# Performance work log

Hardware: AMD Instinct MI355X
Metric: run time of the kernel (lower is better)

## Reference

```python
import jax, jax.numpy as jnp
import numpy as np

N_HEAD = 8
HID = 256
V_DIM = HID // N_HEAD
IN_CH = 3
OUT_CH = 1
N_BLOCKS = 4
BATCH = 4
N_FULL = 4096
N_LAT = 1024
LOCALITIES = (3.0, 5.0, 5.0, 5.0, 5.0, 3.0)


def _linear(x, w, b):
    # eqx.nn.Linear convention: w is [out, in]
    return x @ w.T + b


def _pos_att(m_dist, x, r, weight, locality):
    # m_dist: [h, Nq, Nk]; x: [b, Nk, HID]; r: [h,1,1]; weight: [h, HID, V_DIM]
    scale = jnp.tan(0.25 * jnp.pi * (1 - 1e-07) * (1 + jnp.sin(r)))  # [h,1,1]
    sd = m_dist * scale  # [h, Nq, Nk]
    if locality <= 100:
        thr = jnp.percentile(sd, locality, axis=-1, keepdims=True)
        sd = jnp.where(sd <= thr, sd, jnp.inf)
    att = jax.nn.softmax(-sd, axis=-1)  # [h, Nq, Nk]
    value = jnp.einsum('bnj,hjk->bhnk', x, weight)  # [b, h, Nk, V_DIM]
    out = jnp.einsum('hjn,bhnk->bhjk', att, value)  # [b, h, Nq, V_DIM]
    out = out.transpose(0, 2, 1, 3).reshape(out.shape[0], out.shape[2], -1)  # [b, Nq, HID]
    return jax.nn.gelu(out)


def setup_inputs():
    key = jax.random.key(0)
    ks = jax.random.split(key, 16)
    def nrm(k, shape, scale=1.0):
        return jax.random.normal(k, shape, dtype=jnp.float32) * scale
    inv = float(1.0 / np.sqrt(HID))
    return {
        'x': nrm(ks[0], (BATCH, N_FULL, IN_CH)),
        'm_dist_down': jax.random.uniform(ks[1], (N_HEAD, N_LAT, N_FULL), dtype=jnp.float32),
        'm_dist_blocks': jax.random.uniform(ks[2], (N_BLOCKS, N_HEAD, N_LAT, N_LAT), dtype=jnp.float32),
        'm_dist_up': jax.random.uniform(ks[3], (N_HEAD, N_FULL, N_LAT), dtype=jnp.float32),
        'en_w': nrm(ks[4], (HID, IN_CH), float(1.0 / np.sqrt(IN_CH))),
        'en_b': jnp.zeros((HID,), jnp.float32),
        'down_r': nrm(ks[5], (N_HEAD, 1, 1)),
        'down_w': nrm(ks[6], (N_HEAD, HID, V_DIM), inv),
        'pa_r': nrm(ks[7], (N_BLOCKS, N_HEAD, 1, 1)),
        'pa_w': nrm(ks[8], (N_BLOCKS, N_HEAD, HID, V_DIM), inv),
        'mlp1_w': nrm(ks[9], (N_BLOCKS, HID, HID), inv),
        'mlp1_b': jnp.zeros((N_BLOCKS, HID), jnp.float32),
        'mlp2_w': nrm(ks[10], (N_BLOCKS, HID, HID), inv),
        'mlp2_b': jnp.zeros((N_BLOCKS, HID), jnp.float32),
        'res_w': nrm(ks[11], (N_BLOCKS, HID, HID), inv),
        'res_b': jnp.zeros((N_BLOCKS, HID), jnp.float32),
        'up_r': nrm(ks[12], (N_HEAD, 1, 1)),
        'up_w': nrm(ks[13], (N_HEAD, HID, V_DIM), inv),
        'de1_w': nrm(ks[14], (HID, HID), inv),
        'de1_b': jnp.zeros((HID,), jnp.float32),
        'de2_w': nrm(ks[15], (OUT_CH, HID), inv),
        'de2_b': jnp.zeros((OUT_CH,), jnp.float32),
    }


def reference(x, m_dist_down, m_dist_blocks, m_dist_up, en_w, en_b, down_r, down_w,
              pa_r, pa_w, mlp1_w, mlp1_b, mlp2_w, mlp2_b, res_w, res_b,
              up_r, up_w, de1_w, de1_b, de2_w, de2_b):
    # Encoder: lift + downsampling position-attention
    h = jax.nn.gelu(_linear(x, en_w, en_b))  # [b, N_FULL, HID]
    h = _pos_att(m_dist_down, h, down_r, down_w, LOCALITIES[0])  # [b, N_LAT, HID]
    # Processor blocks: PA -> MLP, plus linear residual, gelu
    for i in range(N_BLOCKS):
        pa = _pos_att(m_dist_blocks[i], h, pa_r[i], pa_w[i], LOCALITIES[1 + i])
        mlp = _linear(jax.nn.gelu(_linear(pa, mlp1_w[i], mlp1_b[i])), mlp2_w[i], mlp2_b[i])
        h = jax.nn.gelu(mlp + _linear(h, res_w[i], res_b[i]))
    # Decoder: upsampling position-attention + projection
    h = _pos_att(m_dist_up, h, up_r, up_w, LOCALITIES[-1])  # [b, N_FULL, HID]
    h = jax.nn.gelu(_linear(h, de1_w, de1_b))
    return _linear(h, de2_w, de2_b)  # [b, N_FULL, OUT_CH]
```

## Files before the change

kernel.cpp:

```cpp
#include <hip/hip_runtime.h>
#include <math.h>


typedef short bf16x8 __attribute__((ext_vector_type(8)));
typedef float f32x4 __attribute__((ext_vector_type(4)));

__device__ __forceinline__ float gelu_f(float x) {
  float x3 = x * x * x;
  float inner = x + 0.044715f * x3;
  float t = tanhf(0.7978845608028654f * inner);
  return x * (0.5f * (1.0f + t));
}

__device__ __forceinline__ unsigned short f2bf(float x) {
  union { float f; unsigned u; } v; v.f = x;
  return (unsigned short)((v.u + 0x7fffu + ((v.u >> 16) & 1u)) >> 16);
}
__device__ __forceinline__ float bf2f(unsigned short b) {
  union { unsigned u; float f; } v; v.u = ((unsigned)b) << 16; return v.f;
}
__device__ __forceinline__ void store_bf(unsigned short* hi, unsigned short* lo,
                                         size_t i, float v) {
  unsigned short h = f2bf(v);
  hi[i] = h;
  lo[i] = f2bf(v - bf2f(h));
}

struct PrepArgs {
  const float *mlp1, *mlp2, *res, *de1, *down, *pa, *up;
  const float *down_r, *pa_r, *up_r;
  unsigned short *rm_hi, *rm_lo, *val_hi, *val_lo;
  float* scales;
};
__global__ __launch_bounds__(256) void k_prep(PrepArgs p) {
  if (blockIdx.x == 4864) {
    int t = threadIdx.x;
    if (t >= 48) return;
    float rv;
    if (t < 8) rv = p.down_r[t];
    else if (t < 40) rv = p.pa_r[t - 8];
    else rv = p.up_r[t - 40];
    double rd = (double)rv;
    float s1 = (float)sin(rd);
    float u = 1.0f + s1;
    float vc = (float)(0.7853981633974483 * (1.0 - 1e-7));
    float wf = vc * u;
    p.scales[t] = (float)tan((double)wf);
    return;
  }
  int i = blockIdx.x * 256 + threadIdx.x;
  if (i < 851968) {
    const float* src; int off;
    if (i < 262144)      { src = p.mlp1; off = i; }
    else if (i < 524288) { src = p.mlp2; off = i - 262144; }
    else if (i < 786432) { src = p.res;  off = i - 524288; }
    else                 { src = p.de1;  off = i - 786432; }
    float x = src[off];
    store_bf(p.rm_hi, p.rm_lo, i, x);
  } else if (i < 1245184) {
    int ii = i - 851968;
    const float* src; int off;
    if (ii < 65536)       { src = p.down; off = ii; }
    else if (ii < 327680) { src = p.pa;   off = ii - 65536; }
    else                  { src = p.up;   off = ii - 327680; }
    int m = off >> 16, rem = off & 65535;
    int o = rem >> 8, j = rem & 255;
    float x = src[(size_t)m * 65536 + (o >> 5) * 8192 + j * 32 + (o & 31)];
    store_bf(p.val_hi, p.val_lo, ii, x);
  }
}

__global__ __launch_bounds__(256) void k_lift(const float* __restrict__ x,
                                              const float* __restrict__ w,
                                              const float* __restrict__ b,
                                              unsigned short* __restrict__ ohi,
                                              unsigned short* __restrict__ olo) {
  int gid = blockIdx.x * 256 + threadIdx.x;
  int m = gid >> 8, o = gid & 255;
  float a0 = x[m * 3 + 0], a1 = x[m * 3 + 1], a2 = x[m * 3 + 2];
  float acc = a0 * w[o * 3 + 0] + a1 * w[o * 3 + 1] + a2 * w[o * 3 + 2] + b[o];
  store_bf(ohi, olo, gid, gelu_f(acc));
}

template <int ACT, int ADDRES, int OBF16>
__global__ __launch_bounds__(256) void k_gemm(
    const unsigned short* __restrict__ Ahi, const unsigned short* __restrict__ Alo,
    const unsigned short* __restrict__ Whi, const unsigned short* __restrict__ Wlo,
    const float* __restrict__ bias, const float* __restrict__ D,
    float* __restrict__ C, unsigned short* __restrict__ Chi,
    unsigned short* __restrict__ Clo) {
  int t = threadIdx.x;
  int w = t >> 6, l = t & 63;
  int m0 = blockIdx.x * 64 + (w >> 1) * 32;
  int o0 = blockIdx.y * 64 + (w & 1) * 32;
  int fr = l & 15, fq = l >> 4;
  f32x4 acc[2][2] = {};
  size_t a0 = (size_t)(m0 + fr) * 256 + fq * 8;
  size_t a1 = a0 + 16 * 256;
  size_t b0 = (size_t)(o0 + fr) * 256 + fq * 8;
  size_t b1 = b0 + 16 * 256;
  for (int ks = 0; ks < 8; ++ks) {
    int k0 = ks * 32;
    bf16x8 A0h = *(const bf16x8*)(Ahi + a0 + k0);
    bf16x8 A0l = *(const bf16x8*)(Alo + a0 + k0);
    bf16x8 A1h = *(const bf16x8*)(Ahi + a1 + k0);
    bf16x8 A1l = *(const bf16x8*)(Alo + a1 + k0);
    bf16x8 B0h = *(const bf16x8*)(Whi + b0 + k0);
    bf16x8 B0l = *(const bf16x8*)(Wlo + b0 + k0);
    bf16x8 B1h = *(const bf16x8*)(Whi + b1 + k0);
    bf16x8 B1l = *(const bf16x8*)(Wlo + b1 + k0);
#define MFMA4(ACC, AH, AL, BH, BL)                                            \
  ACC = __builtin_amdgcn_mfma_f32_16x16x32_bf16(AH, BH, ACC, 0, 0, 0);        \
  ACC = __builtin_amdgcn_mfma_f32_16x16x32_bf16(AH, BL, ACC, 0, 0, 0);        \
  ACC = __builtin_amdgcn_mfma_f32_16x16x32_bf16(AL, BH, ACC, 0, 0, 0);        \
  ACC = __builtin_amdgcn_mfma_f32_16x16x32_bf16(AL, BL, ACC, 0, 0, 0);
    MFMA4(acc[0][0], A0h, A0l, B0h, B0l)
    MFMA4(acc[0][1], A0h, A0l, B1h, B1l)
    MFMA4(acc[1][0], A1h, A1l, B0h, B0l)
    MFMA4(acc[1][1], A1h, A1l, B1h, B1l)
#undef MFMA4
  }
  float bb[2];
  bb[0] = bias ? bias[o0 + fr] : 0.0f;
  bb[1] = bias ? bias[o0 + 16 + fr] : 0.0f;
#pragma unroll
  for (int i = 0; i < 2; ++i) {
#pragma unroll
    for (int jx = 0; jx < 2; ++jx) {
      int col = o0 + jx * 16 + fr;
#pragma unroll
      for (int r = 0; r < 4; ++r) {
        int rowi = m0 + i * 16 + fq * 4 + r;
        size_t oidx = (size_t)rowi * 256 + col;
        float v = acc[i][jx][r] + bb[jx];
        if (ADDRES) v += D[oidx];
        if (ACT) v = gelu_f(v);
        if (OBF16) store_bf(Chi, Clo, oidx, v);
        else C[oidx] = v;
      }
    }
  }
}

template <int N, int CAP, int MW>
__global__ __launch_bounds__(256, MW) void k_wselpv(
    const float* __restrict__ mdist, const float* __restrict__ scales,
    int sc_off, int Nq, int k_lo, float hw, float lw, float frac,
    const float* __restrict__ V, int Nk,
    unsigned short* __restrict__ out_hi, unsigned short* __restrict__ out_lo) {
  constexpr int CH = N / 256;
  constexpr int SMAX = (CAP + 63) / 64;
  __shared__ float cv[4][CAP];
  __shared__ int ci[4][CAP];
  __shared__ int ccnt[4];
  __shared__ float svsel[4][2];
  __shared__ float swin[4][32];

  int tid = threadIdx.x;
  int w = tid >> 6, l = tid & 63;
  int row = blockIdx.x * 4 + w;
  int h = row / Nq, j = row - h * Nq;
  float scale = scales[sc_off + h];
  const float4* mrow4 = (const float4*)(mdist + (size_t)row * N);

  float lmin = INFINITY, lmax = -INFINITY;
#pragma unroll
  for (int e = 0; e < CH; ++e) {
    float4 v = mrow4[l + 64 * e];
    lmin = fminf(lmin, fminf(fminf(v.x, v.y), fminf(v.z, v.w)));
    lmax = fmaxf(lmax, fmaxf(fmaxf(v.x, v.y), fmaxf(v.z, v.w)));
  }
#pragma unroll
  for (int off = 32; off > 0; off >>= 1) {
    lmin = fminf(lmin, __shfl_xor(lmin, off));
    lmax = fmaxf(lmax, __shfl_xor(lmax, off));
  }
  float rmin = lmin, rmax = lmax;

  int K = 0;
  float inv_total = 1.0f;
  if (rmax > rmin) {
    float range = rmax - rmin;
    float margin = fmaxf(fabsf(rmax) * 1e-6f, 1e-30f);
    float rtop = rmax + margin;
    float wtop = rmin + range * frac;
    if (!(wtop > rmin)) wtop = rtop;
    float v_lo = rmin, v_hi = rmin;
    int count = 0;
    float xv[SMAX];
    for (int it = 0; it < 20; ++it) {
      if (l == 0) ccnt[w] = 0;
#pragma unroll
      for (int e = 0; e < CH; ++e) {
        float4 v = mrow4[l + 64 * e];
        int i0 = 4 * (l + 64 * e);
        if (v.x < wtop) { int p = atomicAdd(&ccnt[w], 1); if (p < CAP) { cv[w][p] = v.x; ci[w][p] = i0; } }
        if (v.y < wtop) { int p = atomicAdd(&ccnt[w], 1); if (p < CAP) { cv[w][p] = v.y; ci[w][p] = i0 + 1; } }
        if (v.z < wtop) { int p = atomicAdd(&ccnt[w], 1); if (p < CAP) { cv[w][p] = v.z; ci[w][p] = i0 + 2; } }
        if (v.w < wtop) { int p = atomicAdd(&ccnt[w], 1); if (p < CAP) { cv[w][p] = v.w; ci[w][p] = i0 + 3; } }
      }
      count = ccnt[w];
      if (count < k_lo + 2) { wtop = fminf(rmin + (wtop - rmin) * 3.0f, rtop); continue; }
      if (count > CAP)      { wtop = rmin + (wtop - rmin) * 0.6f; continue; }

#pragma unroll
      for (int s = 0; s < SMAX; ++s) {
        int slot = l + 64 * s;
        xv[s] = (slot < count) ? cv[w][slot] : INFINITY;
      }
      float wlo = rmin, whi = wtop;
      int rbase = 0, cntw = count;
      int found = 0, degen = 0;
      for (int bs = 0; bs < 32; ++bs) {
        if (cntw <= 24) break;
        float mid = 0.5f * (wlo + whi);
        if (!(mid > wlo && mid < whi)) { degen = 1; break; }
        int c4 = 0;
#pragma unroll
        for (int s = 0; s < SMAX; ++s) c4 += (xv[s] >= wlo && xv[s] < mid) ? 1 : 0;
#pragma unroll
        for (int off = 32; off > 0; off >>= 1) c4 += __shfl_xor(c4, off);
        int rrel = k_lo - rbase;
        if (rrel + 1 < c4) { whi = mid; cntw = c4; }
        else if (rrel >= c4) { wlo = mid; rbase += c4; cntw -= c4; }
        else {
          float mx = -INFINITY, mn = INFINITY;
#pragma unroll
          for (int s = 0; s < SMAX; ++s) {
            float v = xv[s];
            if (v >= wlo && v < mid) mx = fmaxf(mx, v);
            if (v >= mid && v < whi) mn = fminf(mn, v);
          }
#pragma unroll
          for (int off = 32; off > 0; off >>= 1) {
            mx = fmaxf(mx, __shfl_xor(mx, off));
            mn = fminf(mn, __shfl_xor(mn, off));
          }
          v_lo = mx; v_hi = mn; found = 1;
          break;
        }
      }
      if (!found) {
        if (!degen && cntw <= 32) {
          if (l == 0) ccnt[w] = 0;
#pragma unroll
          for (int s = 0; s < SMAX; ++s) {
            float v = xv[s];
            if (v >= wlo && v < whi) {
              int p = atomicAdd(&ccnt[w], 1);
              if (p < 32) swin[w][p] = v;
            }
          }
          int m = ccnt[w];
          if (m > 32) m = 32;
          float myv = (l < m) ? swin[w][l] : INFINITY;
          int clt = 0, ceq = 0;
          for (int jj = 0; jj < m; ++jj) {
            float y = swin[w][jj];
            clt += (y < myv) ? 1 : 0;
            ceq += (y == myv) ? 1 : 0;
          }
          int rr = k_lo - rbase;
          if (l < m) {
            if (clt <= rr && rr < clt + ceq) svsel[w][0] = myv;
            if (clt <= rr + 1 && rr + 1 < clt + ceq) svsel[w][1] = myv;
          }
          v_lo = svsel[w][0];
          v_hi = svsel[w][1];
        } else {
          int clt[SMAX], ceq[SMAX];
#pragma unroll
          for (int s = 0; s < SMAX; ++s) { clt[s] = 0; ceq[s] = 0; }
          for (int jj = 0; jj < count; ++jj) {
            float y = cv[w][jj];
#pragma unroll
            for (int s = 0; s < SMAX; ++s) {
              clt[s] += (y < xv[s]) ? 1 : 0;
              ceq[s] += (y == xv[s]) ? 1 : 0;
            }
          }
#pragma unroll
          for (int s = 0; s < SMAX; ++s) {
            int slot = l + 64 * s;
            if (slot < count) {
              if (clt[s] <= k_lo && k_lo < clt[s] + ceq[s]) svsel[w][0] = xv[s];
              if (clt[s] <= k_lo + 1 && k_lo + 1 < clt[s] + ceq[s]) svsel[w][1] = xv[s];
            }
          }
          v_lo = svsel[w][0];
          v_hi = svsel[w][1];
        }
      }
      float vlos0 = __fmul_rn(v_lo, scale);
      float vhis0 = __fmul_rn(v_hi, scale);
      float thr0 = __fadd_rn(__fmul_rn(vlos0, lw), __fmul_rn(vhis0, hw));
      if (__fmul_rn(wtop, scale) <= thr0) {
        wtop = fminf(rmin + (wtop - rmin) * 3.0f, rtop);
        continue;
      }
      break;
    }

    float vlos = __fmul_rn(v_lo, scale);
    float vhis = __fmul_rn(v_hi, scale);
    float thr = __fadd_rn(__fmul_rn(vlos, lw), __fmul_rn(vhis, hw));
    float rmins = __fmul_rn(rmin, scale);

    int oi[SMAX]; int kp[SMAX];
#pragma unroll
    for (int s = 0; s < SMAX; ++s) {
      int slot = l + 64 * s;
      oi[s] = 0; kp[s] = 0;
      if (slot < count) {
        oi[s] = ci[w][slot];
        kp[s] = (__fmul_rn(xv[s], scale) <= thr) ? 1 : 0;
      }
    }
    int base = 0;
    float lsum = 0.0f;
    unsigned long long mlt = (l == 0) ? 0ull : (~0ull >> (64 - l));
#pragma unroll
    for (int s = 0; s < SMAX; ++s) {
      unsigned long long bal = __ballot(kp[s] != 0);
      int pos = base + (int)__popcll(bal & mlt);
      if (kp[s]) {
        float e0 = expf(__fsub_rn(rmins, __fmul_rn(xv[s], scale)));
        cv[w][pos] = e0;
        ci[w][pos] = oi[s];
        lsum += e0;
      }
      base += (int)__popcll(bal);
    }
    K = base;
#pragma unroll
    for (int off = 32; off > 0; off >>= 1) lsum += __shfl_xor(lsum, off);
    inv_total = 1.0f / lsum;
  } else {
    K = 0;
    inv_total = 1.0f / (float)Nk;
  }

  int b = l >> 4, c4 = (l & 15) * 2;
  int hcol = h * 32 + c4;
  const float* Vb = V + (size_t)b * Nk * 256;
  float acc0 = 0.0f, acc1 = 0.0f;
  if (K > 0) {
    for (int e = 0; e < K; ++e) {
      float we = cv[w][e];
      int n = ci[w][e];
      const float2 vv = *(const float2*)(Vb + (size_t)n * 256 + hcol);
      acc0 = fmaf(we, vv.x, acc0);
      acc1 = fmaf(we, vv.y, acc1);
    }
  } else {
    for (int n = 0; n < Nk; ++n) {
      const float2 vv = *(const float2*)(Vb + (size_t)n * 256 + hcol);
      acc0 += vv.x;
      acc1 += vv.y;
    }
  }
  size_t oidx = ((size_t)b * Nq + j) * 256 + hcol;
  store_bf(out_hi, out_lo, oidx, gelu_f(acc0 * inv_total));
  store_bf(out_hi, out_lo, oidx + 1, gelu_f(acc1 * inv_total));
}

__global__ __launch_bounds__(256) void k_de2(const float* __restrict__ A,
                                             const float* __restrict__ w,
                                             const float* __restrict__ b,
                                             float* __restrict__ out) {
  int t = threadIdx.x;
  int row = blockIdx.x * 4 + (t >> 6);
  int lane = t & 63;
  const float* ar = A + (size_t)row * 256;
  float s = 0.0f;
  for (int i = lane; i < 256; i += 64) s = fmaf(ar[i], w[i], s);
#pragma unroll
  for (int off = 32; off > 0; off >>= 1) s += __shfl_down(s, off);
  if (lane == 0) out[row] = s + b[0];
}

struct SelParams { int k_lo; float hw, lw, frac; };
static SelParams sel_params(double q, int N) {
  SelParams p;
  float idx_q = (float)(q / 100.0);
  float pos = idx_q * (float)(N - 1);
  float lo = floorf(pos);
  p.k_lo = (int)lo;
  p.hw = pos - lo;
  p.lw = 1.0f - p.hw;
  float need = (float)(p.k_lo + 2);
  p.frac = (need + 6.0f * sqrtf(need) + 8.0f) / (float)N;
  return p;
}

extern "C" void kernel_launch(void* const* d_in, const int* in_sizes, int n_in,
                              void* d_out, int out_size, void* d_ws, size_t ws_size,
                              hipStream_t stream) {
  const float* x      = (const float*)d_in[0];
  const float* mdd    = (const float*)d_in[1];
  const float* mdb    = (const float*)d_in[2];
  const float* mdu    = (const float*)d_in[3];
  const float* en_w   = (const float*)d_in[4];
  const float* en_b   = (const float*)d_in[5];
  const float* down_r = (const float*)d_in[6];
  const float* down_w = (const float*)d_in[7];
  const float* pa_r   = (const float*)d_in[8];
  const float* pa_w   = (const float*)d_in[9];
  const float* mlp1_w = (const float*)d_in[10];
  const float* mlp1_b = (const float*)d_in[11];
  const float* mlp2_w = (const float*)d_in[12];
  const float* mlp2_b = (const float*)d_in[13];
  const float* res_w  = (const float*)d_in[14];
  const float* res_b  = (const float*)d_in[15];
  const float* up_r   = (const float*)d_in[16];
  const float* up_w   = (const float*)d_in[17];
  const float* de1_w  = (const float*)d_in[18];
  const float* de1_b  = (const float*)d_in[19];
  const float* de2_w  = (const float*)d_in[20];
  const float* de2_b  = (const float*)d_in[21];
  float* out = (float*)d_out;
  char* base = (char*)d_ws;

  float* val               = (float*)base;
  float* t2                = (float*)(base + 16777216);
  unsigned short* hfull_hi = (unsigned short*)(base + 20971520);
  unsigned short* hfull_lo = (unsigned short*)(base + 29360128);
  unsigned short* paout_hi = (unsigned short*)(base + 37748736);
  unsigned short* paout_lo = (unsigned short*)(base + 46137344);
  unsigned short* hlat_hi  = (unsigned short*)(base + 54525952);
  unsigned short* hlat_lo  = (unsigned short*)(base + 56623104);
  unsigned short* t1_hi    = (unsigned short*)(base + 58720256);
  unsigned short* t1_lo    = (unsigned short*)(base + 60817408);
  unsigned short* wrm_hi   = (unsigned short*)(base + 62914560);
  unsigned short* wrm_lo   = (unsigned short*)(base + 64618496);
  unsigned short* wval_hi  = (unsigned short*)(base + 66322432);
  unsigned short* wval_lo  = (unsigned short*)(base + 67108864);
  float* scales            = (float*)(base + 67895296);

  PrepArgs pa;
  pa.mlp1 = mlp1_w; pa.mlp2 = mlp2_w; pa.res = res_w; pa.de1 = de1_w;
  pa.down = down_w; pa.pa = pa_w; pa.up = up_w;
  pa.down_r = down_r; pa.pa_r = pa_r; pa.up_r = up_r;
  pa.rm_hi = wrm_hi; pa.rm_lo = wrm_lo; pa.val_hi = wval_hi; pa.val_lo = wval_lo;
  pa.scales = scales;
  k_prep<<<4865, 256, 0, stream>>>(pa);

  k_lift<<<16384, 256, 0, stream>>>(x, en_w, en_b, hfull_hi, hfull_lo);

  SelParams pd = sel_params(3.0, 4096);
  k_gemm<0, 0, 0><<<dim3(256, 4), 256, 0, stream>>>(
      hfull_hi, hfull_lo, wval_hi, wval_lo, nullptr, nullptr, val, nullptr, nullptr);
  k_wselpv<4096, 256, 4><<<2048, 256, 0, stream>>>(
      mdd, scales, 0, 1024, pd.k_lo, pd.hw, pd.lw, pd.frac, val, 4096, hlat_hi, hlat_lo);

  SelParams pb = sel_params(5.0, 1024);
  for (int i = 0; i < 4; i++) {
    k_gemm<0, 0, 0><<<dim3(64, 4), 256, 0, stream>>>(
        hlat_hi, hlat_lo, wval_hi + 65536 + i * 65536, wval_lo + 65536 + i * 65536,
        nullptr, nullptr, val, nullptr, nullptr);
    k_wselpv<1024, 256, 8><<<2048, 256, 0, stream>>>(
        mdb + (size_t)i * 8388608, scales, 8 + i * 8, 1024, pb.k_lo, pb.hw, pb.lw,
        pb.frac, val, 1024, paout_hi, paout_lo);
    k_gemm<1, 0, 1><<<dim3(64, 4), 256, 0, stream>>>(
        paout_hi, paout_lo, wrm_hi + i * 65536, wrm_lo + i * 65536,
        mlp1_b + i * 256, nullptr, nullptr, t1_hi, t1_lo);
    k_gemm<0, 0, 0><<<dim3(64, 4), 256, 0, stream>>>(
        hlat_hi, hlat_lo, wrm_hi + 524288 + i * 65536, wrm_lo + 524288 + i * 65536,
        res_b + i * 256, nullptr, t2, nullptr, nullptr);
    k_gemm<1, 1, 1><<<dim3(64, 4), 256, 0, stream>>>(
        t1_hi, t1_lo, wrm_hi + 262144 + i * 65536, wrm_lo + 262144 + i * 65536,
        mlp2_b + i * 256, t2, nullptr, hlat_hi, hlat_lo);
  }

  SelParams pu = sel_params(3.0, 1024);
  k_gemm<0, 0, 0><<<dim3(64, 4), 256, 0, stream>>>(
      hlat_hi, hlat_lo, wval_hi + 327680, wval_lo + 327680, nullptr, nullptr,
      val, nullptr, nullptr);
  k_wselpv<1024, 192, 8><<<8192, 256, 0, stream>>>(
      mdu, scales, 40, 4096, pu.k_lo, pu.hw, pu.lw, pu.frac, val, 1024,
      paout_hi, paout_lo);

  k_gemm<1, 0, 0><<<dim3(256, 4), 256, 0, stream>>>(
      paout_hi, paout_lo, wrm_hi + 786432, wrm_lo + 786432, de1_b, nullptr,
      val, nullptr, nullptr);
  k_de2<<<4096, 256, 0, stream>>>(val, de2_w, de2_b, out);
}
```

Measured before the change: 566.7 us.

## Fuse residual and MLP2 GEMMs; merge min/max scan with candidate collection in selection

Result: faster. 521.7 us (-8.0%).

```diff
diff --git a/kernel.cpp b/kernel.cpp
--- a/kernel.cpp
+++ b/kernel.cpp
@@ -99,6 +99,11 @@
   size_t a1 = a0 + 16 * 256;
   size_t b0 = (size_t)(o0 + fr) * 256 + fq * 8;
   size_t b1 = b0 + 16 * 256;
+#define MFMA4(ACC, AH, AL, BH, BL)                                            \
+  ACC = __builtin_amdgcn_mfma_f32_16x16x32_bf16(AH, BH, ACC, 0, 0, 0);        \
+  ACC = __builtin_amdgcn_mfma_f32_16x16x32_bf16(AH, BL, ACC, 0, 0, 0);        \
+  ACC = __builtin_amdgcn_mfma_f32_16x16x32_bf16(AL, BH, ACC, 0, 0, 0);        \
+  ACC = __builtin_amdgcn_mfma_f32_16x16x32_bf16(AL, BL, ACC, 0, 0, 0);
   for (int ks = 0; ks < 8; ++ks) {
     int k0 = ks * 32;
     bf16x8 A0h = *(const bf16x8*)(Ahi + a0 + k0);
@@ -109,16 +114,10 @@
     bf16x8 B0l = *(const bf16x8*)(Wlo + b0 + k0);
     bf16x8 B1h = *(const bf16x8*)(Whi + b1 + k0);
     bf16x8 B1l = *(const bf16x8*)(Wlo + b1 + k0);
-#define MFMA4(ACC, AH, AL, BH, BL)                                            \
-  ACC = __builtin_amdgcn_mfma_f32_16x16x32_bf16(AH, BH, ACC, 0, 0, 0);        \
-  ACC = __builtin_amdgcn_mfma_f32_16x16x32_bf16(AH, BL, ACC, 0, 0, 0);        \
-  ACC = __builtin_amdgcn_mfma_f32_16x16x32_bf16(AL, BH, ACC, 0, 0, 0);        \
-  ACC = __builtin_amdgcn_mfma_f32_16x16x32_bf16(AL, BL, ACC, 0, 0, 0);
     MFMA4(acc[0][0], A0h, A0l, B0h, B0l)
     MFMA4(acc[0][1], A0h, A0l, B1h, B1l)
     MFMA4(acc[1][0], A1h, A1l, B0h, B0l)
     MFMA4(acc[1][1], A1h, A1l, B1h, B1l)
-#undef MFMA4
   }
   float bb[2];
   bb[0] = bias ? bias[o0 + fr] : 0.0f;
@@ -137,6 +136,73 @@
         if (ACT) v = gelu_f(v);
         if (OBF16) store_bf(Chi, Clo, oidx, v);
         else C[oidx] = v;
+      }
+    }
+  }
+}
+
+__global__ __launch_bounds__(256) void k_gemm2(
+    const unsigned short* __restrict__ A1hi, const unsigned short* __restrict__ A1lo,
+    const unsigned short* __restrict__ W1hi, const unsigned short* __restrict__ W1lo,
+    const unsigned short* __restrict__ A2hi, const unsigned short* __restrict__ A2lo,
+    const unsigned short* __restrict__ W2hi, const unsigned short* __restrict__ W2lo,
+    const float* __restrict__ b1, const float* __restrict__ b2,
+    unsigned short* __restrict__ Chi, unsigned short* __restrict__ Clo) {
+  int t = threadIdx.x;
+  int w = t >> 6, l = t & 63;
+  int m0 = blockIdx.x * 64 + (w >> 1) * 32;
+  int o0 = blockIdx.y * 64 + (w & 1) * 32;
+  int fr = l & 15, fq = l >> 4;
+  f32x4 acc[2][2] = {};
+  size_t a0 = (size_t)(m0 + fr) * 256 + fq * 8;
+  size_t a1 = a0 + 16 * 256;
+  size_t b0 = (size_t)(o0 + fr) * 256 + fq * 8;
+  size_t b1o = b0 + 16 * 256;
+  for (int ks = 0; ks < 8; ++ks) {
+    int k0 = ks * 32;
+    {
+      bf16x8 A0h = *(const bf16x8*)(A1hi + a0 + k0);
+      bf16x8 A0l = *(const bf16x8*)(A1lo + a0 + k0);
+      bf16x8 A1h_ = *(const bf16x8*)(A1hi + a1 + k0);
+      bf16x8 A1l_ = *(const bf16x8*)(A1lo + a1 + k0);
+      bf16x8 B0h = *(const bf16x8*)(W1hi + b0 + k0);
+      bf16x8 B0l = *(const bf16x8*)(W1lo + b0 + k0);
+      bf16x8 B1h = *(const bf16x8*)(W1hi + b1o + k0);
+      bf16x8 B1l = *(const bf16x8*)(W1lo + b1o + k0);
+      MFMA4(acc[0][0], A0h, A0l, B0h, B0l)
+      MFMA4(acc[0][1], A0h, A0l, B1h, B1l)
+      MFMA4(acc[1][0], A1h_, A1l_, B0h, B0l)
+      MFMA4(acc[1][1], A1h_, A1l_, B1h, B1l)
+    }
+    {
+      bf16x8 A0h = *(const bf16x8*)(A2hi + a0 + k0);
+      bf16x8 A0l = *(const bf16x8*)(A2lo + a0 + k0);
+      bf16x8 A1h_ = *(const bf16x8*)(A2hi + a1 + k0);
+      bf16x8 A1l_ = *(const bf16x8*)(A2lo + a1 + k0);
+      bf16x8 B0h = *(const bf16x8*)(W2hi + b0 + k0);
+      bf16x8 B0l = *(const bf16x8*)(W2lo + b0 + k0);
+      bf16x8 B1h = *(const bf16x8*)(W2hi + b1o + k0);
+      bf16x8 B1l = *(const bf16x8*)(W2lo + b1o + k0);
+      MFMA4(acc[0][0], A0h, A0l, B0h, B0l)
+      MFMA4(acc[0][1], A0h, A0l, B1h, B1l)
+      MFMA4(acc[1][0], A1h_, A1l_, B0h, B0l)
+      MFMA4(acc[1][1], A1h_, A1l_, B1h, B1l)
+    }
+  }
+#undef MFMA4
+  float bb[2];
+  bb[0] = b1[o0 + fr] + b2[o0 + fr];
+  bb[1] = b1[o0 + 16 + fr] + b2[o0 + 16 + fr];
+#pragma unroll
+  for (int i = 0; i < 2; ++i) {
+#pragma unroll
+    for (int jx = 0; jx < 2; ++jx) {
+      int col = o0 + jx * 16 + fr;
+#pragma unroll
+      for (int r = 0; r < 4; ++r) {
+        int rowi = m0 + i * 16 + fq * 4 + r;
+        size_t oidx = (size_t)rowi * 256 + col;
+        store_bf(Chi, Clo, oidx, gelu_f(acc[i][jx][r] + bb[jx]));
       }
     }
   }
@@ -163,12 +229,28 @@
   float scale = scales[sc_off + h];
   const float4* mrow4 = (const float4*)(mdist + (size_t)row * N);
 
+  float4 s0 = mrow4[l];
+  float smin = fminf(fminf(s0.x, s0.y), fminf(s0.z, s0.w));
+  float smax = fmaxf(fmaxf(s0.x, s0.y), fmaxf(s0.z, s0.w));
+#pragma unroll
+  for (int off = 32; off > 0; off >>= 1) {
+    smin = fminf(smin, __shfl_xor(smin, off));
+    smax = fmaxf(smax, __shfl_xor(smax, off));
+  }
+  float est = smin + (smax - smin) * frac;
+
+  if (l == 0) ccnt[w] = 0;
   float lmin = INFINITY, lmax = -INFINITY;
-#pragma unroll
+#pragma unroll 4
   for (int e = 0; e < CH; ++e) {
     float4 v = mrow4[l + 64 * e];
     lmin = fminf(lmin, fminf(fminf(v.x, v.y), fminf(v.z, v.w)));
     lmax = fmaxf(lmax, fmaxf(fmaxf(v.x, v.y), fmaxf(v.z, v.w)));
+    int i0 = 4 * (l + 64 * e);
+    if (v.x < est) { int p = atomicAdd(&ccnt[w], 1); if (p < CAP) { cv[w][p] = v.x; ci[w][p] = i0; } }
+    if (v.y < est) { int p = atomicAdd(&ccnt[w], 1); if (p < CAP) { cv[w][p] = v.y; ci[w][p] = i0 + 1; } }
+    if (v.z < est) { int p = atomicAdd(&ccnt[w], 1); if (p < CAP) { cv[w][p] = v.z; ci[w][p] = i0 + 2; } }
+    if (v.w < est) { int p = atomicAdd(&ccnt[w], 1); if (p < CAP) { cv[w][p] = v.w; ci[w][p] = i0 + 3; } }
   }
 #pragma unroll
   for (int off = 32; off > 0; off >>= 1) {
@@ -183,25 +265,44 @@
     float range = rmax - rmin;
     float margin = fmaxf(fabsf(rmax) * 1e-6f, 1e-30f);
     float rtop = rmax + margin;
-    float wtop = rmin + range * frac;
-    if (!(wtop > rmin)) wtop = rtop;
+    float wtop = est;
+    bool have = true;
+    if (!(wtop > rmin)) {
+      wtop = rmin + range * frac;
+      if (!(wtop > rmin)) wtop = rtop;
+      have = false;
+    }
+    int attempt = 0;
     float v_lo = rmin, v_hi = rmin;
     int count = 0;
     float xv[SMAX];
     for (int it = 0; it < 20; ++it) {
-      if (l == 0) ccnt[w] = 0;
-#pragma unroll
-      for (int e = 0; e < CH; ++e) {
-        float4 v = mrow4[l + 64 * e];
-        int i0 = 4 * (l + 64 * e);
-        if (v.x < wtop) { int p = atomicAdd(&ccnt[w], 1); if (p < CAP) { cv[w][p] = v.x; ci[w][p] = i0; } }
-        if (v.y < wtop) { int p = atomicAdd(&ccnt[w], 1); if (p < CAP) { cv[w][p] = v.y; ci[w][p] = i0 + 1; } }
-        if (v.z < wtop) { int p = atomicAdd(&ccnt[w], 1); if (p < CAP) { cv[w][p] = v.z; ci[w][p] = i0 + 2; } }
-        if (v.w < wtop) { int p = atomicAdd(&ccnt[w], 1); if (p < CAP) { cv[w][p] = v.w; ci[w][p] = i0 + 3; } }
+      if (!have) {
+        if (l == 0) ccnt[w] = 0;
+#pragma unroll 4
+        for (int e = 0; e < CH; ++e) {
+          float4 v = mrow4[l + 64 * e];
+          int i0 = 4 * (l + 64 * e);
+          if (v.x < wtop) { int p = atomicAdd(&ccnt[w], 1); if (p < CAP) { cv[w][p] = v.x; ci[w][p] = i0; } }
+          if (v.y < wtop) { int p = atomicAdd(&ccnt[w], 1); if (p < CAP) { cv[w][p] = v.y; ci[w][p] = i0 + 1; } }
+          if (v.z < wtop) { int p = atomicAdd(&ccnt[w], 1); if (p < CAP) { cv[w][p] = v.z; ci[w][p] = i0 + 2; } }
+          if (v.w < wtop) { int p = atomicAdd(&ccnt[w], 1); if (p < CAP) { cv[w][p] = v.w; ci[w][p] = i0 + 3; } }
+        }
+        have = true;
       }
       count = ccnt[w];
-      if (count < k_lo + 2) { wtop = fminf(rmin + (wtop - rmin) * 3.0f, rtop); continue; }
-      if (count > CAP)      { wtop = rmin + (wtop - rmin) * 0.6f; continue; }
+      if (count < k_lo + 2) {
+        wtop = (attempt == 0) ? (rmin + range * frac)
+                              : fminf(rmin + (wtop - rmin) * 3.0f, rtop);
+        if (!(wtop > rmin)) wtop = rtop;
+        attempt++; have = false; continue;
+      }
+      if (count > CAP) {
+        float fw = rmin + range * frac;
+        float sw = rmin + (wtop - rmin) * 0.6f;
+        wtop = (attempt == 0) ? fminf(fw, sw) : sw;
+        attempt++; have = false; continue;
+      }
 
 #pragma unroll
       for (int s = 0; s < SMAX; ++s) {
@@ -267,6 +368,7 @@
           }
           v_lo = svsel[w][0];
           v_hi = svsel[w][1];
+          if (l == 0) ccnt[w] = count;
         } else {
           int clt[SMAX], ceq[SMAX];
 #pragma unroll
@@ -296,7 +398,7 @@
       float thr0 = __fadd_rn(__fmul_rn(vlos0, lw), __fmul_rn(vhis0, hw));
       if (__fmul_rn(wtop, scale) <= thr0) {
         wtop = fminf(rmin + (wtop - rmin) * 3.0f, rtop);
-        continue;
+        attempt++; have = false; continue;
       }
       break;
     }
@@ -422,13 +524,14 @@
   char* base = (char*)d_ws;
 
   float* val               = (float*)base;
-  float* t2                = (float*)(base + 16777216);
+  unsigned short* hB_hi    = (unsigned short*)(base + 16777216);
+  unsigned short* hB_lo    = (unsigned short*)(base + 18874368);
   unsigned short* hfull_hi = (unsigned short*)(base + 20971520);
   unsigned short* hfull_lo = (unsigned short*)(base + 29360128);
   unsigned short* paout_hi = (unsigned short*)(base + 37748736);
   unsigned short* paout_lo = (unsigned short*)(base + 46137344);
-  unsigned short* hlat_hi  = (unsigned short*)(base + 54525952);
-  unsigned short* hlat_lo  = (unsigned short*)(base + 56623104);
+  unsigned short* hA_hi    = (unsigned short*)(base + 54525952);
+  unsigned short* hA_lo    = (unsigned short*)(base + 56623104);
   unsigned short* t1_hi    = (unsigned short*)(base + 58720256);
   unsigned short* t1_lo    = (unsigned short*)(base + 60817408);
   unsigned short* wrm_hi   = (unsigned short*)(base + 62914560);
@@ -451,12 +554,16 @@
   k_gemm<0, 0, 0><<<dim3(256, 4), 256, 0, stream>>>(
       hfull_hi, hfull_lo, wval_hi, wval_lo, nullptr, nullptr, val, nullptr, nullptr);
   k_wselpv<4096, 256, 4><<<2048, 256, 0, stream>>>(
-      mdd, scales, 0, 1024, pd.k_lo, pd.hw, pd.lw, pd.frac, val, 4096, hlat_hi, hlat_lo);
+      mdd, scales, 0, 1024, pd.k_lo, pd.hw, pd.lw, pd.frac, val, 4096, hA_hi, hA_lo);
 
   SelParams pb = sel_params(5.0, 1024);
   for (int i = 0; i < 4; i++) {
+    unsigned short* in_hi  = (i & 1) ? hB_hi : hA_hi;
+    unsigned short* in_lo  = (i & 1) ? hB_lo : hA_lo;
+    unsigned short* out_hi = (i & 1) ? hA_hi : hB_hi;
+    unsigned short* out_lo = (i & 1) ? hA_lo : hB_lo;
     k_gemm<0, 0, 0><<<dim3(64, 4), 256, 0, stream>>>(
-        hlat_hi, hlat_lo, wval_hi + 65536 + i * 65536, wval_lo + 65536 + i * 65536,
+        in_hi, in_lo, wval_hi + 65536 + i * 65536, wval_lo + 65536 + i * 65536,
         nullptr, nullptr, val, nullptr, nullptr);
     k_wselpv<1024, 256, 8><<<2048, 256, 0, stream>>>(
         mdb + (size_t)i * 8388608, scales, 8 + i * 8, 1024, pb.k_lo, pb.hw, pb.lw,
@@ -464,17 +571,15 @@
     k_gemm<1, 0, 1><<<dim3(64, 4), 256, 0, stream>>>(
         paout_hi, paout_lo, wrm_hi + i * 65536, wrm_lo + i * 65536,
         mlp1_b + i * 256, nullptr, nullptr, t1_hi, t1_lo);
-    k_gemm<0, 0, 0><<<dim3(64, 4), 256, 0, stream>>>(
-        hlat_hi, hlat_lo, wrm_hi + 524288 + i * 65536, wrm_lo + 524288 + i * 65536,
-        res_b + i * 256, nullptr, t2, nullptr, nullptr);
-    k_gemm<1, 1, 1><<<dim3(64, 4), 256, 0, stream>>>(
+    k_gemm2<<<dim3(64, 4), 256, 0, stream>>>(
         t1_hi, t1_lo, wrm_hi + 262144 + i * 65536, wrm_lo + 262144 + i * 65536,
-        mlp2_b + i * 256, t2, nullptr, hlat_hi, hlat_lo);
+        in_hi, in_lo, wrm_hi + 524288 + i * 65536, wrm_lo + 524288 + i * 65536,
+        mlp2_b + i * 256, res_b + i * 256, out_hi, out_lo);
   }
 
   SelParams pu = sel_params(3.0, 1024);
   k_gemm<0, 0, 0><<<dim3(64, 4), 256, 0, stream>>>(
-      hlat_hi, hlat_lo, wval_hi + 327680, wval_lo + 327680, nullptr, nullptr,
+      hA_hi, hA_lo, wval_hi + 327680, wval_lo + 327680, nullptr, nullptr,
       val, nullptr, nullptr);
   k_wselpv<1024, 192, 8><<<8192, 256, 0, stream>>>(
       mdu, scales, 40, 4096, pu.k_lo, pu.hw, pu.lw, pu.frac, val, 1024,
```
